# Performance work log

Measured on AMD Instinct MI355X. Metric: run time of the kernel, lower is better.

## Reference

```python
import jax, jax.numpy as jnp
import numpy as np

# pywt db8 decomposition low-pass filter (dec_lo), 16 taps
DB8_DEC_LO = jnp.array([
    -0.00011747678400228192, 0.0006754494059985568, -0.0003917403729959771,
    -0.00487035299301066, 0.008746094047015655, 0.013981027917015516,
    -0.04408825393106472, -0.01736930100202211, 0.128747426620186,
    0.00047248457399797254, -0.2840155429624281, -0.015829105256023893,
    0.5853546836548691, 0.6756307362980128, 0.3128715909144659,
    0.05441584224308161], dtype=jnp.float32)


def _dwt_lo_last(x, filt):
    """pywt single-level low-pass DWT along last axis, mode='symmetric'.
    out[m] = sum_k filt[k] * x_ext[2m + 1 + (flen-1) - k]; len = (n+flen-1)//2.
    Implemented as: symmetric-pad by flen-1, drop first sample, stride-2
    correlation with the reversed filter (== true convolution)."""
    flen = filt.shape[0]
    pad = [(0, 0)] * (x.ndim - 1) + [(flen - 1, flen - 1)]
    xe = jnp.pad(x, pad, mode='symmetric')[..., 1:]
    lead = x.shape[:-1]
    y = jax.lax.conv_general_dilated(
        xe.reshape(int(np.prod(lead)), 1, xe.shape[-1]),
        filt[::-1].reshape(1, 1, flen),
        window_strides=(2,), padding='VALID')
    return y.reshape(*lead, -1)


def dwt2_ll(x, filt):
    """LL band of pywt.dwt2 on x[..., H, W] (separable: rows then cols)."""
    y = _dwt_lo_last(x, filt)            # low-pass + downsample along W
    y = jnp.swapaxes(y, -1, -2)
    y = _dwt_lo_last(y, filt)            # low-pass + downsample along H
    return jnp.swapaxes(y, -1, -2)


def setup_inputs() -> dict:
    key = jax.random.key(0)
    k1, k2, k3 = jax.random.split(key, 3)
    B, C, H, W = 8, 256, 256, 256
    r = 16
    x = jax.random.normal(k1, (B, C, H, W), dtype=jnp.float32)
    W1 = jax.random.normal(k2, (C // r, C), dtype=jnp.float32) * (1.0 / np.sqrt(C))
    W2 = jax.random.normal(k3, (C, C // r), dtype=jnp.float32) * (1.0 / np.sqrt(C // r))
    return {"x": x, "W1": W1, "W2": W2}


def reference(x, W1, W2):
    # x: [B, C, H, W]
    ll = dwt2_ll(x, DB8_DEC_LO)                    # [B, C, (H+15)//2, (W+15)//2]
    y = jnp.mean(ll, axis=(2, 3))                  # adaptive avg pool to 1x1 -> [B, C]
    h = jax.nn.relu(y @ W1.T)                      # [B, C/r]
    w = jax.nn.sigmoid(h @ W2.T)                   # [B, C]
    return x * w[:, :, None, None]
```

## Files before the change

kernel.cpp:

```cpp
#include <hip/hip_runtime.h>
#include <math.h>


#define BATCH 8
#define CH    256
#define HW    256
#define BC    (BATCH*CH)
#define LL    135

struct AVec { float a[256]; };

__global__ __launch_bounds__(256) void wa_reduce(const float* __restrict__ x,
                                                 float* __restrict__ s, AVec av) {
    const int bc = blockIdx.x;
    const float4* __restrict__ xr = (const float4*)(x + (size_t)bc * (HW * HW));
    const int t  = threadIdx.x;
    const int cg = t & 63;
    const int rg = t >> 6;
    float4 acc = make_float4(0.f, 0.f, 0.f, 0.f);
    #pragma unroll 4
    for (int i = rg * 64; i < rg * 64 + 64; ++i) {
        float4 v = xr[(size_t)i * 64 + cg];
        const float ai = av.a[i];
        acc.x = fmaf(ai, v.x, acc.x);
        acc.y = fmaf(ai, v.y, acc.y);
        acc.z = fmaf(ai, v.z, acc.z);
        acc.w = fmaf(ai, v.w, acc.w);
    }
    float partial = acc.x * av.a[4*cg+0] + acc.y * av.a[4*cg+1]
                  + acc.z * av.a[4*cg+2] + acc.w * av.a[4*cg+3];
    #pragma unroll
    for (int off = 32; off > 0; off >>= 1)
        partial += __shfl_down(partial, off, 64);
    __shared__ float wsum[4];
    if (cg == 0) wsum[rg] = partial;
    __syncthreads();
    if (t == 0) s[bc] = wsum[0] + wsum[1] + wsum[2] + wsum[3];
}

__global__ __launch_bounds__(256) void wa_mlp(const float* __restrict__ s,
                                              const float* __restrict__ W1,
                                              const float* __restrict__ W2,
                                              float* __restrict__ wout) {
    const int b = blockIdx.x;
    const int c = threadIdx.x;
    __shared__ float y[256];
    __shared__ float h[16];
    y[c] = s[b * 256 + c] * (1.0f / (135.0f * 135.0f));
    __syncthreads();
    if (c < 16) {
        float acc = 0.f;
        for (int k = 0; k < 256; ++k) acc = fmaf(y[k], W1[c * 256 + k], acc);
        h[c] = fmaxf(acc, 0.f);
    }
    __syncthreads();
    float acc = 0.f;
    #pragma unroll
    for (int j = 0; j < 16; ++j) acc = fmaf(h[j], W2[c * 16 + j], acc);
    wout[b * 256 + c] = 1.f / (1.f + expf(-acc));
}

__global__ __launch_bounds__(256) void wa_scale(const float4* __restrict__ x,
                                                const float* __restrict__ w,
                                                float4* __restrict__ out) {
    const size_t i = (size_t)blockIdx.x * 256 + threadIdx.x;
    const float wv = w[i >> 14];
    float4 v = x[i];
    v.x *= wv; v.y *= wv; v.z *= wv; v.w *= wv;
    out[i] = v;
}

extern "C" void kernel_launch(void* const* d_in, const int* in_sizes, int n_in,
                              void* d_out, int out_size, void* d_ws, size_t ws_size,
                              hipStream_t stream) {
    const float* x  = (const float*)d_in[0];
    const float* W1 = (const float*)d_in[1];
    const float* W2 = (const float*)d_in[2];
    float* out = (float*)d_out;

    float* s  = (float*)d_ws;
    float* wv = s + BC;

    static const double DB8[16] = {
        -0.00011747678400228192, 0.0006754494059985568, -0.0003917403729959771,
        -0.00487035299301066, 0.008746094047015655, 0.013981027917015516,
        -0.04408825393106472, -0.01736930100202211, 0.128747426620186,
        0.00047248457399797254, -0.2840155429624281, -0.015829105256023893,
        0.5853546836548691, 0.6756307362980128, 0.3128715909144659,
        0.05441584224308161};
    double tmp[256];
    for (int j = 0; j < 256; ++j) tmp[j] = 0.0;
    for (int m = 0; m < LL; ++m) {
        for (int t = 0; t < 16; ++t) {
            int i = 2 * m + t - 14;
            int j = (i < 0) ? (-1 - i) : ((i >= 256) ? (511 - i) : i);
            tmp[j] += DB8[15 - t];
        }
    }
    AVec av;
    for (int j = 0; j < 256; ++j) av.a[j] = (float)tmp[j];

    wa_reduce<<<BC, 256, 0, stream>>>(x, s, av);
    wa_mlp<<<BATCH, 256, 0, stream>>>(s, W1, W2, wv);
    const int n4 = BATCH * CH * HW * HW / 4;
    wa_scale<<<n4 / 256, 256, 0, stream>>>((const float4*)x, wv, (float4*)out);
}
```

Measured before the change: 930.1 us.

## Fuse reduce, MLP and scale into per-batch pipelined launches

Replaces the three kernels with one fused kernel launched once per batch step. Each launch reduces batch b, split into four row-chunk blocks per channel, while also recomputing the MLP gate and scaling batch b-1 using double-buffered partial sums. The aim is to overlap the read-heavy reduction with the read/write-heavy scaling and to drop the separate MLP launch. In exchange it adds nine launches, recomputes the small MLP in every scale block, and uses nontemporal stores for the output.

```diff
diff --git a/kernel.cpp b/kernel.cpp
--- a/kernel.cpp
+++ b/kernel.cpp
@@ -5,69 +5,82 @@
 #define BATCH 8
 #define CH    256
 #define HW    256
-#define BC    (BATCH*CH)
 #define LL    135
+
+typedef float vf4 __attribute__((ext_vector_type(4)));
 
 struct AVec { float a[256]; };
 
-__global__ __launch_bounds__(256) void wa_reduce(const float* __restrict__ x,
-                                                 float* __restrict__ s, AVec av) {
-    const int bc = blockIdx.x;
-    const float4* __restrict__ xr = (const float4*)(x + (size_t)bc * (HW * HW));
-    const int t  = threadIdx.x;
-    const int cg = t & 63;
-    const int rg = t >> 6;
-    float4 acc = make_float4(0.f, 0.f, 0.f, 0.f);
-    #pragma unroll 4
-    for (int i = rg * 64; i < rg * 64 + 64; ++i) {
-        float4 v = xr[(size_t)i * 64 + cg];
-        const float ai = av.a[i];
-        acc.x = fmaf(ai, v.x, acc.x);
-        acc.y = fmaf(ai, v.y, acc.y);
-        acc.z = fmaf(ai, v.z, acc.z);
-        acc.w = fmaf(ai, v.w, acc.w);
+__global__ __launch_bounds__(256) void wa_fused(
+    const float* __restrict__ x, const float* __restrict__ W1,
+    const float* __restrict__ W2, float* __restrict__ out,
+    float* __restrict__ s_part, AVec av, int breduce, int bscale, int nred)
+{
+    const int t = threadIdx.x;
+    __shared__ float ysh[256];
+    __shared__ float hsh[16];
+    __shared__ float wsum[4];
+
+    if ((int)blockIdx.x < nred) {
+        const int c   = blockIdx.x >> 2;
+        const int sub = blockIdx.x & 3;
+        const float4* __restrict__ xr =
+            (const float4*)(x + (((size_t)(breduce * CH + c)) << 16));
+        const int cg = t & 63;
+        const int rg = t >> 6;
+        const int r0 = sub * 64 + rg * 16;
+        float4 acc = make_float4(0.f, 0.f, 0.f, 0.f);
+        #pragma unroll 4
+        for (int i = r0; i < r0 + 16; ++i) {
+            float4 v = xr[(size_t)i * 64 + cg];
+            const float ai = av.a[i];
+            acc.x = fmaf(ai, v.x, acc.x);
+            acc.y = fmaf(ai, v.y, acc.y);
+            acc.z = fmaf(ai, v.z, acc.z);
+            acc.w = fmaf(ai, v.w, acc.w);
+        }
+        float partial = acc.x * av.a[4*cg+0] + acc.y * av.a[4*cg+1]
+                      + acc.z * av.a[4*cg+2] + acc.w * av.a[4*cg+3];
+        #pragma unroll
+        for (int off = 32; off > 0; off >>= 1)
+            partial += __shfl_down(partial, off, 64);
+        if (cg == 0) wsum[rg] = partial;
+        __syncthreads();
+        if (t == 0)
+            s_part[(breduce & 1) * 1024 + c * 4 + sub] =
+                wsum[0] + wsum[1] + wsum[2] + wsum[3];
+        return;
     }
-    float partial = acc.x * av.a[4*cg+0] + acc.y * av.a[4*cg+1]
-                  + acc.z * av.a[4*cg+2] + acc.w * av.a[4*cg+3];
+
+    const int sb = blockIdx.x - nred;
+    const float* __restrict__ sp = s_part + (bscale & 1) * 1024;
+    ysh[t] = (sp[t*4+0] + sp[t*4+1] + sp[t*4+2] + sp[t*4+3])
+             * (1.0f / (135.0f * 135.0f));
+    __syncthreads();
+    const int j = t >> 4, l16 = t & 15;
+    float hp = 0.f;
+    for (int k = l16; k < 256; k += 16) hp = fmaf(ysh[k], W1[j*256 + k], hp);
     #pragma unroll
-    for (int off = 32; off > 0; off >>= 1)
-        partial += __shfl_down(partial, off, 64);
-    __shared__ float wsum[4];
-    if (cg == 0) wsum[rg] = partial;
+    for (int off = 8; off > 0; off >>= 1) hp += __shfl_xor(hp, off, 16);
+    if (l16 == 0) hsh[j] = fmaxf(hp, 0.f);
     __syncthreads();
-    if (t == 0) s[bc] = wsum[0] + wsum[1] + wsum[2] + wsum[3];
-}
+    const int c_s = sb >> 3;
+    float g = 0.f;
+    #pragma unroll
+    for (int jj = 0; jj < 16; ++jj) g = fmaf(hsh[jj], W2[c_s*16 + jj], g);
+    g = 1.f / (1.f + expf(-g));
 
-__global__ __launch_bounds__(256) void wa_mlp(const float* __restrict__ s,
-                                              const float* __restrict__ W1,
-                                              const float* __restrict__ W2,
-                                              float* __restrict__ wout) {
-    const int b = blockIdx.x;
-    const int c = threadIdx.x;
-    __shared__ float y[256];
-    __shared__ float h[16];
-    y[c] = s[b * 256 + c] * (1.0f / (135.0f * 135.0f));
-    __syncthreads();
-    if (c < 16) {
-        float acc = 0.f;
-        for (int k = 0; k < 256; ++k) acc = fmaf(y[k], W1[c * 256 + k], acc);
-        h[c] = fmaxf(acc, 0.f);
+    const vf4* __restrict__ x4 = (const vf4*)x;
+    vf4* __restrict__ o4 = (vf4*)out;
+    const size_t base4 = ((size_t)bscale << 22)
+                       + ((size_t)sb << 11) + t;
+    #pragma unroll
+    for (int k = 0; k < 8; ++k) {
+        const size_t i = base4 + ((size_t)k << 8);
+        vf4 v = x4[i];
+        v *= g;
+        __builtin_nontemporal_store(v, o4 + i);
     }
-    __syncthreads();
-    float acc = 0.f;
-    #pragma unroll
-    for (int j = 0; j < 16; ++j) acc = fmaf(h[j], W2[c * 16 + j], acc);
-    wout[b * 256 + c] = 1.f / (1.f + expf(-acc));
-}
-
-__global__ __launch_bounds__(256) void wa_scale(const float4* __restrict__ x,
-                                                const float* __restrict__ w,
-                                                float4* __restrict__ out) {
-    const size_t i = (size_t)blockIdx.x * 256 + threadIdx.x;
-    const float wv = w[i >> 14];
-    float4 v = x[i];
-    v.x *= wv; v.y *= wv; v.z *= wv; v.w *= wv;
-    out[i] = v;
 }
 
 extern "C" void kernel_launch(void* const* d_in, const int* in_sizes, int n_in,
@@ -77,9 +90,7 @@
     const float* W1 = (const float*)d_in[1];
     const float* W2 = (const float*)d_in[2];
     float* out = (float*)d_out;
-
-    float* s  = (float*)d_ws;
-    float* wv = s + BC;
+    float* s_part = (float*)d_ws;
 
     static const double DB8[16] = {
         -0.00011747678400228192, 0.0006754494059985568, -0.0003917403729959771,
@@ -89,19 +100,22 @@
         0.5853546836548691, 0.6756307362980128, 0.3128715909144659,
         0.05441584224308161};
     double tmp[256];
-    for (int j = 0; j < 256; ++j) tmp[j] = 0.0;
+    for (int jj = 0; jj < 256; ++jj) tmp[jj] = 0.0;
     for (int m = 0; m < LL; ++m) {
-        for (int t = 0; t < 16; ++t) {
-            int i = 2 * m + t - 14;
-            int j = (i < 0) ? (-1 - i) : ((i >= 256) ? (511 - i) : i);
-            tmp[j] += DB8[15 - t];
+        for (int tt = 0; tt < 16; ++tt) {
+            int i = 2 * m + tt - 14;
+            int jj = (i < 0) ? (-1 - i) : ((i >= 256) ? (511 - i) : i);
+            tmp[jj] += DB8[15 - tt];
         }
     }
     AVec av;
-    for (int j = 0; j < 256; ++j) av.a[j] = (float)tmp[j];
+    for (int jj = 0; jj < 256; ++jj) av.a[jj] = (float)tmp[jj];
 
-    wa_reduce<<<BC, 256, 0, stream>>>(x, s, av);
-    wa_mlp<<<BATCH, 256, 0, stream>>>(s, W1, W2, wv);
-    const int n4 = BATCH * CH * HW * HW / 4;
-    wa_scale<<<n4 / 256, 256, 0, stream>>>((const float4*)x, wv, (float4*)out);
+    for (int b = 0; b <= BATCH; ++b) {
+        const int nred = (b < BATCH) ? 1024 : 0;
+        const int nsc  = (b >= 1)    ? 2048 : 0;
+        if (nred + nsc == 0) continue;
+        wa_fused<<<nred + nsc, 256, 0, stream>>>(
+            x, W1, W2, out, s_part, av, b, b - 1, nred);
+    }
 }
```

Result: no change. 921.0 us (-1.0%).
